# Optimization experiments

Hardware: AMD Instinct MI355X
Metric: run time of the kernel (lower is better)

## Reference

```python
import jax, jax.numpy as jnp
import numpy as np
import math

NEG = -1e32
B, S, D, H, DFF, L = 16, 512, 1024, 8, 4096, 3
DK = D // H


def layernorm(x, g, b, eps=1e-5):
    mu = x.mean(-1, keepdims=True)
    var = ((x - mu) ** 2).mean(-1, keepdims=True)
    return (x - mu) / jnp.sqrt(var + eps) * g + b


def gen_dam(alphas, E, bmask):
    # alphas, E: [H, S, 2]; hard gumbel-softmax with straight-through
    Hh, Ss, _ = alphas.shape
    g = -jnp.log(E + 1e-5)
    y_soft = jax.nn.softmax(alphas + g, axis=-1)  # tau = 1
    idx = jnp.argmax(y_soft, axis=-1)
    y_hard = jax.nn.one_hot(idx, 2, dtype=y_soft.dtype)
    m = y_hard - jax.lax.stop_gradient(y_soft) + y_soft
    m = jnp.broadcast_to(m[:, :, 0:1], (Hh, Ss, Ss))
    m = jnp.triu(m)
    m = jnp.rot90(m, 1, axes=(1, 2))
    i = jnp.arange(Ss)[:, None]
    j = jnp.arange(Ss)[None, :]
    src = jnp.clip(j - i, 0, Ss - 1)
    shifted = m[:, jnp.arange(Ss)[:, None], src]  # mask_tri[:, i, j] = m[:, i, j - i]
    mask_tri = jnp.where(j >= i, shifted, 0.0)
    masks = mask_tri + jnp.swapaxes(jnp.triu(mask_tri, 1), 1, 2)
    masks = jnp.triu(masks, bmask)
    return masks


def attention(q, k, v, src_mask, dam, zero_pad, gammas):
    # q,k,v: [B,H,S,dk]; src_mask: [S,S] bool; dam: [H,S,S] bool
    dk = q.shape[-1]
    Ss = q.shape[2]
    scores = jnp.einsum('bhqd,bhkd->bhqk', q, k) / math.sqrt(dk)
    damb = dam[None]          # [1,H,S,S]
    smb = src_mask[None, None]  # [1,1,S,S]
    # NOTE: faithful to the torch code, where the first masked_fill(mask==0)
    # result is overwritten - only dam masks the first softmax.
    sc = jnp.where(damb, scores, NEG)
    sc = jax.nn.softmax(sc, axis=-1)
    sc = sc * smb.astype(sc.dtype) * damb.astype(sc.dtype)
    distcum = jnp.cumsum(sc, axis=-1)
    disttot = jnp.sum(sc, axis=-1, keepdims=True)
    pos = jnp.abs(jnp.arange(Ss)[None, :] - jnp.arange(Ss)[:, None]).astype(scores.dtype)
    dist = jnp.sqrt(jnp.clip((disttot - distcum) * pos[None, None], 0.0, None))
    dist = jax.lax.stop_gradient(dist)
    gamma = -jax.nn.softplus(gammas)[None]  # [1,H,1,1]
    te = jnp.clip(jnp.exp(dist * gamma), 1e-5, 1e5)
    scores = scores * te
    scores = jnp.where(smb, scores, NEG)
    scores = jnp.where(damb, scores, NEG)
    scores = jax.nn.softmax(scores, axis=-1)
    if zero_pad:
        scores = scores.at[:, :, 0, :].set(0.0)
    return jnp.einsum('bhqk,bhkd->bhqd', scores, v)


def transformer_layer(bmask, query, key, values, apply_pos, p):
    Bb, Ss, Dd = query.shape
    Hh = p['gammas'].shape[0]
    dam = gen_dam(p['alphas'], p['E'], bmask) == 0
    src_mask = jnp.triu(jnp.ones((Ss, Ss), jnp.int32), bmask) == 0
    k = (key @ p['kW'].T + p['kb']).reshape(Bb, Ss, Hh, -1).transpose(0, 2, 1, 3)
    q = (query @ p['kW'].T + p['kb']).reshape(Bb, Ss, Hh, -1).transpose(0, 2, 1, 3)  # kq_same
    v = (values @ p['vW'].T + p['vb']).reshape(Bb, Ss, Hh, -1).transpose(0, 2, 1, 3)
    att = attention(q, k, v, src_mask, dam, bmask == 0, p['gammas'])
    concat = att.transpose(0, 2, 1, 3).reshape(Bb, Ss, Dd)
    q2 = concat @ p['oW'].T + p['ob']
    x = layernorm(query + q2, p['ln1_g'], p['ln1_b'])
    if apply_pos:
        ff = jax.nn.relu(x @ p['w1'].T + p['b1']) @ p['w2'].T + p['b2']
        x = layernorm(x + ff, p['ln2_g'], p['ln2_b'])
    return x


def setup_inputs() -> dict:
    key = jax.random.key(0)
    ks = jax.random.split(key, 16)
    sc = 0.02
    return {
        'q_embed_data': jax.random.normal(ks[0], (B, S, D), jnp.float32),
        'qa_embed_data': jax.random.normal(ks[1], (B, S, D), jnp.float32),
        'kW': sc * jax.random.normal(ks[2], (L, D, D), jnp.float32),
        'kb': jnp.zeros((L, D), jnp.float32),
        'vW': sc * jax.random.normal(ks[3], (L, D, D), jnp.float32),
        'vb': jnp.zeros((L, D), jnp.float32),
        'oW': sc * jax.random.normal(ks[4], (L, D, D), jnp.float32),
        'ob': jnp.zeros((L, D), jnp.float32),
        'gammas': 0.5 * jax.random.normal(ks[5], (L, H, 1, 1), jnp.float32),
        'alphas': 0.001 * jax.random.normal(ks[6], (L, H, S, 2), jnp.float32),
        'ln1_g': jnp.ones((L, D), jnp.float32),
        'ln1_b': jnp.zeros((L, D), jnp.float32),
        'w1': sc * jax.random.normal(ks[7], (L, DFF, D), jnp.float32),
        'b1': jnp.zeros((L, DFF), jnp.float32),
        'w2': sc * jax.random.normal(ks[8], (L, D, DFF), jnp.float32),
        'b2': jnp.zeros((L, D), jnp.float32),
        'ln2_g': jnp.ones((L, D), jnp.float32),
        'ln2_b': jnp.zeros((L, D), jnp.float32),
        'gumbel_E': jax.random.exponential(ks[9], (L, H, S, 2), jnp.float32),
    }


def reference(q_embed_data, qa_embed_data, kW, kb, vW, vb, oW, ob, gammas,
              alphas, ln1_g, ln1_b, w1, b1, w2, b2, ln2_g, ln2_b, gumbel_E):
    def P(l):
        return {'kW': kW[l], 'kb': kb[l], 'vW': vW[l], 'vb': vb[l],
                'oW': oW[l], 'ob': ob[l], 'gammas': gammas[l], 'alphas': alphas[l],
                'ln1_g': ln1_g[l], 'ln1_b': ln1_b[l], 'w1': w1[l], 'b1': b1[l],
                'w2': w2[l], 'b2': b2[l], 'ln2_g': ln2_g[l], 'ln2_b': ln2_b[l],
                'E': gumbel_E[l]}
    # blocks_1: self-attention over answer embedding (mask=1)
    y = transformer_layer(1, qa_embed_data, qa_embed_data, qa_embed_data, True, P(0))
    # blocks_2: self-attn on question emb (no FFN), then cross-attn into y
    x = transformer_layer(1, q_embed_data, q_embed_data, q_embed_data, False, P(1))
    x = transformer_layer(0, x, x, y, True, P(2))
    return x
```

## Files before the change

### kernel.cpp

```cpp
#include <hip/hip_runtime.h>
#include <math.h>

#define NEGV -1e32f

typedef __bf16 bf16_t;
typedef _Float16 f16_t;
typedef __bf16 bf16x8 __attribute__((ext_vector_type(8)));
typedef __bf16 bf16x4 __attribute__((ext_vector_type(4)));
typedef _Float16 f16x8 __attribute__((ext_vector_type(8)));
typedef float floatx4 __attribute__((ext_vector_type(4)));

static __device__ __forceinline__ float fexp(float x) { return __expf(x); }
#if __has_builtin(__builtin_amdgcn_sqrtf)
static __device__ __forceinline__ float fsqrt(float x) { return __builtin_amdgcn_sqrtf(x); }
#else
static __device__ __forceinline__ float fsqrt(float x) { return sqrtf(x); }
#endif
#if __has_builtin(__builtin_amdgcn_rcpf)
static __device__ __forceinline__ float frcp(float x) { return __builtin_amdgcn_rcpf(x); }
#else
static __device__ __forceinline__ float frcp(float x) { return 1.0f / x; }
#endif

static __device__ __forceinline__ float wave_sum(float v) {
#pragma unroll
  for (int d = 32; d > 0; d >>= 1) v += __shfl_xor(v, d, 64);
  return v;
}
static __device__ __forceinline__ float wave_max(float v) {
#pragma unroll
  for (int d = 32; d > 0; d >>= 1) v = fmaxf(v, __shfl_xor(v, d, 64));
  return v;
}

static __device__ __forceinline__ void gl2lds16(const bf16_t* g, bf16_t* l) {
  __builtin_amdgcn_global_load_lds((__attribute__((address_space(1))) void*)(void*)g,
                                   (__attribute__((address_space(3))) void*)l, 16, 0, 0);
}

template <int WM, int WN, int FM, int FN, int BIAS_MODE, bool RELU, int OUT_MODE>
__global__ __launch_bounds__(WM * WN * 64) void gemm_db(
    const bf16_t* __restrict__ A, long lda, long a_so, long a_si,
    const bf16_t* __restrict__ B, long ldb, long b_so, long b_si,
    void* __restrict__ Cv, long ldc, long c_so, long c_si,
    const float* __restrict__ bias, int zdiv, int K, float alpha)
{
  constexpr int THREADS = WM * WN * 64;
  constexpr int BM = WM * FM * 16;
  constexpr int BN = WN * FN * 16;
  constexpr int RR = THREADS / 8;
  constexpr int RA = BM / RR;
  constexpr int RB = BN / RR;
  constexpr int NSTG = RA + RB;
  constexpr int MG = (FM >= 8) ? 2 : 1;
  constexpr int MSUB = FM / MG;
  constexpr int PH = 2 * MG;
  extern __shared__ bf16_t smem[];
  bf16_t* const Asb = smem;
  bf16_t* const Bsb = smem + 2 * (BM * 64);

  const int tid = threadIdx.x;
  const int wave = tid >> 6;
  const int lane = tid & 63;
  const int wm = wave / WN;
  const int wn = wave % WN;
  const int z = blockIdx.z;
  const long zo = z / zdiv;
  const long zi = z % zdiv;
  A += zo * a_so + zi * a_si;
  B += zo * b_so + zi * b_si;
  const long m0 = (long)blockIdx.x * BM;
  const long n0 = (long)blockIdx.y * BN;

  const int srow = tid >> 3;
  const int scol = ((tid & 7) ^ (srow & 7)) * 8;
  const bf16_t* gA = A + (m0 + srow) * lda + scol;
  const bf16_t* gB = B + (n0 + srow) * ldb + scol;
  const int lofs = wave * 512;

  floatx4 acc[FM][FN] = {};
  const int lr = lane & 15;
  const int kg = lane >> 4;
  const int NT = K >> 6;

  auto stage_round = [&](int q, long ko, int dstbuf) {
    if (q < RA)
      gl2lds16(gA + (long)(q * RR) * lda + ko,
               Asb + dstbuf * (BM * 64) + lofs + q * RR * 64);
    else
      gl2lds16(gB + (long)((q - RA) * RR) * ldb + ko,
               Bsb + dstbuf * (BN * 64) + lofs + (q - RA) * RR * 64);
  };

#pragma unroll
  for (int q = 0; q < NSTG; ++q) stage_round(q, 0, 0);

  for (int t = 0; t < NT; ++t) {
    const int buf = t & 1;
    const bool pf = (t + 1 < NT);
    const long ko = (long)(t + 1) * 64;
    if (pf) {
#pragma unroll
      for (int q = 0; q < 2; ++q) stage_round(q, ko, buf ^ 1);
      asm volatile("s_waitcnt vmcnt(2)" ::: "memory");
    } else {
      asm volatile("s_waitcnt vmcnt(0)" ::: "memory");
    }
    __builtin_amdgcn_s_barrier();
    __builtin_amdgcn_sched_barrier(0);
    const bf16_t* __restrict__ Ab = Asb + buf * (BM * 64);
    const bf16_t* __restrict__ Bb = Bsb + buf * (BN * 64);
#pragma unroll
    for (int h = 0; h < 2; ++h) {
      const int slot = ((h * 4 + kg) ^ (lr & 7)) * 8;
      bf16x8 bfr[FN];
#pragma unroll
      for (int g = 0; g < MG; ++g) {
        const int pi = h * MG + g;
        bf16x8 af[MSUB];
#pragma unroll
        for (int m = 0; m < MSUB; ++m)
          af[m] = *(const bf16x8*)(Ab + (wm * (FM * 16) + (g * MSUB + m) * 16 + lr) * 64 + slot);
        if (g == 0) {
#pragma unroll
          for (int n = 0; n < FN; ++n)
            bfr[n] = *(const bf16x8*)(Bb + (wn * (FN * 16) + n * 16 + lr) * 64 + slot);
        }
        if (pf) {
          const int q0 = 2 + pi * 6 / PH;
          const int q1 = 2 + (pi + 1) * 6 / PH;
#pragma unroll
          for (int q = q0; q < q1; ++q) stage_round(q, ko, buf ^ 1);
        }
        asm volatile("s_waitcnt lgkmcnt(0)" ::: "memory");
        __builtin_amdgcn_sched_barrier(0);
        __builtin_amdgcn_s_setprio(1);
#pragma unroll
        for (int m = 0; m < MSUB; ++m)
#pragma unroll
          for (int n = 0; n < FN; ++n)
            acc[g * MSUB + m][n] =
                __builtin_amdgcn_mfma_f32_16x16x32_bf16(af[m], bfr[n], acc[g * MSUB + m][n], 0, 0, 0);
        __builtin_amdgcn_s_setprio(0);
        __builtin_amdgcn_sched_barrier(0);
        __builtin_amdgcn_s_barrier();
      }
    }
  }

  const long coff = zo * c_so + zi * c_si;
  const int q4 = (lane >> 4) * 4;
#pragma unroll
  for (int m = 0; m < FM; ++m) {
#pragma unroll
    for (int n = 0; n < FN; ++n) {
#pragma unroll
      for (int r = 0; r < 4; ++r) {
        const long row = m0 + wm * (FM * 16) + m * 16 + q4 + r;
        const long col = n0 + wn * (FN * 16) + n * 16 + lr;
        float v = acc[m][n][r] * alpha;
        if (BIAS_MODE == 1) v += bias[col];
        if (BIAS_MODE == 2) v += bias[row];
        if (RELU) v = fmaxf(v, 0.0f);
        const long idx = coff + row * ldc + col;
        if (OUT_MODE == 1)      ((bf16_t*)Cv)[idx] = (bf16_t)v;
        else if (OUT_MODE == 2) ((f16_t*)Cv)[idx]  = (f16_t)v;
        else                    ((float*)Cv)[idx]  = v;
      }
    }
  }
}

template <int BIAS_MODE, bool RELU, int OUT_MODE>
__global__ __launch_bounds__(256) void gemm_bt(
    const bf16_t* __restrict__ A, long lda, long a_so, long a_si,
    const bf16_t* __restrict__ B, long ldb, long b_so, long b_si,
    void* __restrict__ Cv, long ldc, long c_so, long c_si,
    const float* __restrict__ bias, int zdiv, int K, float alpha)
{
  __shared__ bf16_t As[8192];
  __shared__ bf16_t Bs[8192];
  const int tid = threadIdx.x;
  const int wave = tid >> 6;
  const int lane = tid & 63;
  const int wr = wave >> 1;
  const int wc = wave & 1;
  const int z = blockIdx.z;
  const long zo = z / zdiv;
  const long zi = z % zdiv;
  A += zo * a_so + zi * a_si;
  B += zo * b_so + zi * b_si;
  const long m0 = (long)blockIdx.x * 128;
  const long n0 = (long)blockIdx.y * 128;

  const int srow = tid >> 3;
  const int scol = ((tid & 7) ^ (srow & 7)) * 8;
  const bf16_t* gA = A + (m0 + srow) * lda + scol;
  const bf16_t* gB = B + (n0 + srow) * ldb + scol;
  bf16_t* lA = As + wave * 512;
  bf16_t* lB = Bs + wave * 512;

  floatx4 acc[4][4] = {};
  const int lr = lane & 15;
  const int kg = lane >> 4;

  for (int k0 = 0; k0 < K; k0 += 64) {
#pragma unroll
    for (int r = 0; r < 4; ++r) {
      gl2lds16(gA + (long)r * 32 * lda + k0, lA + r * 2048);
      gl2lds16(gB + (long)r * 32 * ldb + k0, lB + r * 2048);
    }
    __syncthreads();
#pragma unroll
    for (int h = 0; h < 2; ++h) {
      const int slot = ((h * 4 + kg) ^ (lr & 7)) * 8;
      bf16x8 af[4], bfr[4];
#pragma unroll
      for (int t = 0; t < 4; ++t) {
        af[t]  = *(const bf16x8*)(As + (wr * 64 + t * 16 + lr) * 64 + slot);
        bfr[t] = *(const bf16x8*)(Bs + (wc * 64 + t * 16 + lr) * 64 + slot);
      }
#pragma unroll
      for (int tm = 0; tm < 4; ++tm)
#pragma unroll
        for (int tn = 0; tn < 4; ++tn)
          acc[tm][tn] = __builtin_amdgcn_mfma_f32_16x16x32_bf16(af[tm], bfr[tn], acc[tm][tn], 0, 0, 0);
    }
    __syncthreads();
  }

  const long coff = zo * c_so + zi * c_si;
  const int q4 = (lane >> 4) * 4;
#pragma unroll
  for (int tm = 0; tm < 4; ++tm) {
#pragma unroll
    for (int tn = 0; tn < 4; ++tn) {
#pragma unroll
      for (int r = 0; r < 4; ++r) {
        const long row = m0 + wr * 64 + tm * 16 + q4 + r;
        const long col = n0 + wc * 64 + tn * 16 + lr;
        float v = acc[tm][tn][r] * alpha;
        if (BIAS_MODE == 1) v += bias[col];
        if (BIAS_MODE == 2) v += bias[row];
        if (RELU) v = fmaxf(v, 0.0f);
        const long idx = coff + row * ldc + col;
        if (OUT_MODE == 1)      ((bf16_t*)Cv)[idx] = (bf16_t)v;
        else if (OUT_MODE == 2) ((f16_t*)Cv)[idx]  = (f16_t)v;
        else                    ((float*)Cv)[idx]  = v;
      }
    }
  }
}

__global__ __launch_bounds__(256) void cast_kernel(const float* __restrict__ in,
                                                   bf16_t* __restrict__ out, long n)
{
  const long i = ((long)blockIdx.x * 256 + threadIdx.x) * 4;
  if (i >= n) return;
  const float4 v = *(const float4*)(in + i);
  bf16x4 o;
  o[0] = (bf16_t)v.x; o[1] = (bf16_t)v.y; o[2] = (bf16_t)v.z; o[3] = (bf16_t)v.w;
  *(bf16x4*)(out + i) = o;
}

__global__ void bbit_kernel(const float* __restrict__ alphas, const float* __restrict__ E,
                            int* __restrict__ bbit, int n)
{
  const int i = blockIdx.x * 256 + threadIdx.x;
  if (i >= n) return;
  const float l0 = alphas[2 * i]     - logf(E[2 * i]     + 1e-5f);
  const float l1 = alphas[2 * i + 1] - logf(E[2 * i + 1] + 1e-5f);
  bbit[i] = (l0 >= l1) ? 1 : 0;
}

template <bool XBF>
__global__ __launch_bounds__(256) void ln_kernel(
    const void* __restrict__ Xv, const float* __restrict__ R,
    const float* __restrict__ g, const float* __restrict__ b,
    float* __restrict__ out32, bf16_t* __restrict__ out16)
{
  const long row = blockIdx.x;
  const int t = threadIdx.x;
  float x0, x1, x2, x3;
  if (XBF) {
    const bf16x4 xv = *(const bf16x4*)((const bf16_t*)Xv + row * 1024 + t * 4);
    x0 = (float)xv[0]; x1 = (float)xv[1]; x2 = (float)xv[2]; x3 = (float)xv[3];
  } else {
    const float4 xv = *(const float4*)((const float*)Xv + row * 1024 + t * 4);
    x0 = xv.x; x1 = xv.y; x2 = xv.z; x3 = xv.w;
  }
  const float4 rv = *(const float4*)(R + row * 1024 + t * 4);
  const float v0 = x0 + rv.x, v1 = x1 + rv.y, v2 = x2 + rv.z, v3 = x3 + rv.w;
  float s  = v0 + v1 + v2 + v3;
  float s2 = v0 * v0 + v1 * v1 + v2 * v2 + v3 * v3;
  s = wave_sum(s); s2 = wave_sum(s2);
  __shared__ float red[8];
  const int wv = t >> 6, lane = t & 63;
  if (lane == 0) { red[wv] = s; red[4 + wv] = s2; }
  __syncthreads();
  s  = red[0] + red[1] + red[2] + red[3];
  s2 = red[4] + red[5] + red[6] + red[7];
  const float mu = s * (1.0f / 1024.0f);
  const float var = s2 * (1.0f / 1024.0f) - mu * mu;
  const float rstd = rsqrtf(var + 1e-5f);
  const float4 gv = *(const float4*)(g + t * 4);
  const float4 bv = *(const float4*)(b + t * 4);
  float4 ov;
  ov.x = (v0 - mu) * rstd * gv.x + bv.x;
  ov.y = (v1 - mu) * rstd * gv.y + bv.y;
  ov.z = (v2 - mu) * rstd * gv.z + bv.z;
  ov.w = (v3 - mu) * rstd * gv.w + bv.w;
  if (out32) *(float4*)(out32 + row * 1024 + t * 4) = ov;
  if (out16) {
    bf16x4 oh;
    oh[0] = (bf16_t)ov.x; oh[1] = (bf16_t)ov.y; oh[2] = (bf16_t)ov.z; oh[3] = (bf16_t)ov.w;
    *(bf16x4*)(out16 + row * 1024 + t * 4) = oh;
  }
}

__global__ __launch_bounds__(256) void attn_mid(
    const f16_t* __restrict__ S, bf16_t* __restrict__ P,
    const int* __restrict__ bbit, const float* __restrict__ gam,
    const int bmask, const int zero_pad)
{
  const int wid = threadIdx.x >> 6;
  const int lane = threadIdx.x & 63;
  const long rowid = (long)blockIdx.x * 4 + wid;
  const int i = (int)(rowid & 511);
  const int h = (int)(rowid >> 9) & 7;
  const f16_t* s = S + rowid * 512;
  const int jb = lane * 8;

  const float gv = gam[h];
  const float gamma = -log1pf(fexp(gv));

  float sv[8];
  {
    const f16x8 a = *(const f16x8*)(s + jb);
#pragma unroll
    for (int u = 0; u < 8; ++u) sv[u] = (float)a[u];
  }
  const int* bb = bbit + h * 512;
  float z[8];
  bool band[8];
  float m1 = NEGV;
#pragma unroll
  for (int u = 0; u < 8; ++u) {
    const int j = jb + u;
    const bool bd = j < i + bmask;
    band[u] = bd;
    int d = j - i; d = d < 0 ? 0 : d;
    const bool allowed = bd || (bb[d] == 0);
    z[u] = allowed ? sv[u] : NEGV;
    m1 = fmaxf(m1, z[u]);
  }
  m1 = wave_max(m1);
  float e[8], es = 0.f;
#pragma unroll
  for (int u = 0; u < 8; ++u) { e[u] = fexp(z[u] - m1); es += e[u]; }
  es = wave_sum(es);
  const float inv1 = frcp(es);

  float c[8];
  float run = 0.f;
#pragma unroll
  for (int u = 0; u < 8; ++u) {
    const float p = band[u] ? e[u] * inv1 : 0.f;
    run += p;
    c[u] = run;
  }
  float x = run;
#pragma unroll
  for (int d = 1; d < 64; d <<= 1) {
    const float y = __shfl_up(x, (unsigned)d, 64);
    if (lane >= d) x += y;
  }
  const float tot = __shfl(x, 63, 64);
  const float ex = x - run;

  float z2[8];
  float m2 = NEGV;
#pragma unroll
  for (int u = 0; u < 8; ++u) {
    const int j = jb + u;
    const float cc = c[u] + ex;
    const float pos = fabsf((float)(i - j));
    const float dist = fsqrt(fmaxf((tot - cc) * pos, 0.f));
    float te = fexp(dist * gamma);
    te = fminf(fmaxf(te, 1e-5f), 1e5f);
    z2[u] = band[u] ? sv[u] * te : NEGV;
    m2 = fmaxf(m2, z2[u]);
  }
  m2 = wave_max(m2);
  float f[8], es2 = 0.f;
#pragma unroll
  for (int u = 0; u < 8; ++u) { f[u] = fexp(z2[u] - m2); es2 += f[u]; }
  es2 = wave_sum(es2);
  const float inv2 = (zero_pad && i == 0) ? 0.f : frcp(es2);
  bf16x8 o;
#pragma unroll
  for (int u = 0; u < 8; ++u) o[u] = (bf16_t)(f[u] * inv2);
  *(bf16x8*)(P + rowid * 512 + jb) = o;
}

extern "C" void kernel_launch(void* const* d_in, const int* in_sizes, int n_in,
                              void* d_out, int out_size, void* d_ws, size_t ws_size,
                              hipStream_t stream)
{
  (void)in_sizes; (void)n_in; (void)out_size; (void)ws_size;
  const float* q_emb  = (const float*)d_in[0];
  const float* qa_emb = (const float*)d_in[1];
  const float* kW = (const float*)d_in[2];
  const float* kb = (const float*)d_in[3];
  const float* vW = (const float*)d_in[4];
  const float* vb = (const float*)d_in[5];
  const float* oW = (const float*)d_in[6];
  const float* ob = (const float*)d_in[7];
  const float* gammas = (const float*)d_in[8];
  const float* alphas = (const float*)d_in[9];
  const float* ln1_g = (const float*)d_in[10];
  const float* ln1_b = (const float*)d_in[11];
  const float* w1 = (const float*)d_in[12];
  const float* b1 = (const float*)d_in[13];
  const float* w2 = (const float*)d_in[14];
  const float* b2 = (const float*)d_in[15];
  const float* ln2_g = (const float*)d_in[16];
  const float* ln2_b = (const float*)d_in[17];
  const float* gumE = (const float*)d_in[18];
  float* outp = (float*)d_out;

  static bool attr_done = false;
  if (!attr_done) {
    attr_done = true;
    (void)hipFuncSetAttribute(reinterpret_cast<const void*>(&gemm_db<2,2,4,4,1,false,1>),
                              hipFuncAttributeMaxDynamicSharedMemorySize, 65536);
    (void)hipFuncSetAttribute(reinterpret_cast<const void*>(&gemm_db<2,2,4,4,2,false,1>),
                              hipFuncAttributeMaxDynamicSharedMemorySize, 65536);
    (void)hipFuncSetAttribute(reinterpret_cast<const void*>(&gemm_db<2,2,4,4,0,false,1>),
                              hipFuncAttributeMaxDynamicSharedMemorySize, 65536);
    (void)hipFuncSetAttribute(reinterpret_cast<const void*>(&gemm_db<2,2,4,4,1,false,0>),
                              hipFuncAttributeMaxDynamicSharedMemorySize, 65536);
    (void)hipFuncSetAttribute(reinterpret_cast<const void*>(&gemm_db<2,4,8,4,1,true,1>),
                              hipFuncAttributeMaxDynamicSharedMemorySize, 131072);
  }

  const size_t MBc = 1ull << 20;
  char* W = (char*)d_ws;
  int*    bbit = (int*)W;
  bf16_t* VB   = (bf16_t*)(W + 1 * MBc);
  bf16_t* XB   = (bf16_t*)(W + 17 * MBc);
  bf16_t* kWb  = (bf16_t*)(W + 33 * MBc);
  bf16_t* vWb  = (bf16_t*)(W + 39 * MBc);
  bf16_t* oWb  = (bf16_t*)(W + 45 * MBc);
  bf16_t* w1b  = (bf16_t*)(W + 51 * MBc);
  bf16_t* w2b  = (bf16_t*)(W + 59 * MBc);
  bf16_t* KQB  = (bf16_t*)(W + 67 * MBc);
  bf16_t* VT   = (bf16_t*)(W + 83 * MBc);
  f16_t*  SSPP = (f16_t*)(W + 99 * MBc);
  bf16_t* PPb  = (bf16_t*)(W + 99 * MBc);
  bf16_t* ATT  = (bf16_t*)(W + 163 * MBc);
  float*  O32  = (float*)(W + 67 * MBc);
  bf16_t* X1B  = (bf16_t*)(W + 99 * MBc);
  bf16_t* H1B  = (bf16_t*)(W + 115 * MBc);

  const long ND = 8388608;

  auto run_layer = [&](int l, const void* Qin, bool qin_bf16, const bf16_t* XBp,
                       const bf16_t* VBp, bool apply_pos, int bmask,
                       float* o32, bf16_t* o16) {
    const bf16_t* kWl = kWb + (long)l * 1048576;
    const bf16_t* vWl = vWb + (long)l * 1048576;
    const bf16_t* oWl = oWb + (long)l * 1048576;
    gemm_db<2,2,4,4,1,false,1><<<dim3(64, 8, 1), dim3(256), 65536, stream>>>(
        XBp, 1024, 0, 0, kWl, 1024, 0, 0, (void*)KQB, 1024, 0, 0,
        kb + l * 1024, 1, 1024, 1.0f);
    gemm_db<2,2,4,4,2,false,1><<<dim3(8, 4, 16), dim3(256), 65536, stream>>>(
        vWl, 1024, 0, 0, VBp, 1024, 524288, 0, (void*)VT, 512, 524288, 0,
        vb + l * 1024, 1, 1024, 1.0f);
    const int zp = (bmask == 0) ? 1 : 0;
    gemm_bt<0, false, 2><<<dim3(4, 4, 128), dim3(256), 0, stream>>>(
        KQB, 1024, 524288, 128, KQB, 1024, 524288, 128,
        (void*)SSPP, 512, 2097152, 262144, nullptr, 8, 128, 0.08838834764831845f);
    attn_mid<<<dim3(16384), dim3(256), 0, stream>>>(
        SSPP, PPb, bbit + l * 4096, gammas + l * 8, bmask, zp);
    gemm_db<2,2,4,4,0,false,1><<<dim3(4, 1, 128), dim3(256), 65536, stream>>>(
        PPb, 512, 2097152, 262144, VT, 512, 524288, 65536,
        (void*)ATT, 1024, 524288, 128, nullptr, 8, 512, 1.0f);
    gemm_db<2,2,4,4,1,false,0><<<dim3(64, 8, 1), dim3(256), 65536, stream>>>(
        ATT, 1024, 0, 0, oWl, 1024, 0, 0, (void*)O32, 1024, 0, 0,
        ob + l * 1024, 1, 1024, 1.0f);
    if (!apply_pos) {
      if (qin_bf16)
        ln_kernel<true><<<dim3(8192), dim3(256), 0, stream>>>(
            Qin, O32, ln1_g + l * 1024, ln1_b + l * 1024, o32, o16);
      else
        ln_kernel<false><<<dim3(8192), dim3(256), 0, stream>>>(
            Qin, O32, ln1_g + l * 1024, ln1_b + l * 1024, o32, o16);
    } else {
      cast_kernel<<<dim3(4096), dim3(256), 0, stream>>>(w1 + (long)l * 4194304, w1b, 4194304);
      cast_kernel<<<dim3(4096), dim3(256), 0, stream>>>(w2 + (long)l * 4194304, w2b, 4194304);
      if (qin_bf16)
        ln_kernel<true><<<dim3(8192), dim3(256), 0, stream>>>(
            Qin, O32, ln1_g + l * 1024, ln1_b + l * 1024, nullptr, X1B);
      else
        ln_kernel<false><<<dim3(8192), dim3(256), 0, stream>>>(
            Qin, O32, ln1_g + l * 1024, ln1_b + l * 1024, nullptr, X1B);
      gemm_db<2,4,8,4,1,true,1><<<dim3(32, 16, 1), dim3(512), 131072, stream>>>(
          X1B, 1024, 0, 0, w1b, 1024, 0, 0, (void*)H1B, 4096, 0, 0,
          b1 + l * 4096, 1, 1024, 1.0f);
      gemm_db<2,2,4,4,1,false,0><<<dim3(64, 8, 1), dim3(256), 65536, stream>>>(
          H1B, 4096, 0, 0, w2b, 4096, 0, 0, (void*)O32, 1024, 0, 0,
          b2 + l * 1024, 1, 4096, 1.0f);
      ln_kernel<true><<<dim3(8192), dim3(256), 0, stream>>>(
          X1B, O32, ln2_g + l * 1024, ln2_b + l * 1024, o32, o16);
    }
  };

  bbit_kernel<<<dim3(48), dim3(256), 0, stream>>>(alphas, gumE, bbit, 12288);
  cast_kernel<<<dim3(3072), dim3(256), 0, stream>>>(kW, kWb, 3145728);
  cast_kernel<<<dim3(3072), dim3(256), 0, stream>>>(vW, vWb, 3145728);
  cast_kernel<<<dim3(3072), dim3(256), 0, stream>>>(oW, oWb, 3145728);

  cast_kernel<<<dim3(8192), dim3(256), 0, stream>>>(qa_emb, XB, ND);
  run_layer(0, qa_emb, false, XB, XB, true, 1, nullptr, VB);
  cast_kernel<<<dim3(8192), dim3(256), 0, stream>>>(q_emb, XB, ND);
  run_layer(1, q_emb, false, XB, XB, false, 1, nullptr, XB);
  run_layer(2, XB, true, XB, VB, true, 0, outp, nullptr);
}
```

Before: 1.099 ms.

## Issue all next-tile loads upfront in gemm_db and reuse it for QK^T

New measurement: 1.125 ms. 2.4% more time.

```diff
diff --git a/kernel.cpp b/kernel.cpp
--- a/kernel.cpp
+++ b/kernel.cpp
@@ -54,7 +54,6 @@
   constexpr int NSTG = RA + RB;
   constexpr int MG = (FM >= 8) ? 2 : 1;
   constexpr int MSUB = FM / MG;
-  constexpr int PH = 2 * MG;
   extern __shared__ bf16_t smem[];
   bf16_t* const Asb = smem;
   bf16_t* const Bsb = smem + 2 * (BM * 64);
@@ -97,12 +96,11 @@
 
   for (int t = 0; t < NT; ++t) {
     const int buf = t & 1;
-    const bool pf = (t + 1 < NT);
-    const long ko = (long)(t + 1) * 64;
-    if (pf) {
-#pragma unroll
-      for (int q = 0; q < 2; ++q) stage_round(q, ko, buf ^ 1);
-      asm volatile("s_waitcnt vmcnt(2)" ::: "memory");
+    if (t + 1 < NT) {
+      const long ko = (long)(t + 1) * 64;
+#pragma unroll
+      for (int q = 0; q < NSTG; ++q) stage_round(q, ko, buf ^ 1);
+      asm volatile("s_waitcnt vmcnt(%0)" :: "n"(NSTG) : "memory");
     } else {
       asm volatile("s_waitcnt vmcnt(0)" ::: "memory");
     }
@@ -116,7 +114,6 @@
       bf16x8 bfr[FN];
 #pragma unroll
       for (int g = 0; g < MG; ++g) {
-        const int pi = h * MG + g;
         bf16x8 af[MSUB];
 #pragma unroll
         for (int m = 0; m < MSUB; ++m)
@@ -126,13 +123,8 @@
           for (int n = 0; n < FN; ++n)
             bfr[n] = *(const bf16x8*)(Bb + (wn * (FN * 16) + n * 16 + lr) * 64 + slot);
         }
-        if (pf) {
-          const int q0 = 2 + pi * 6 / PH;
-          const int q1 = 2 + (pi + 1) * 6 / PH;
-#pragma unroll
-          for (int q = q0; q < q1; ++q) stage_round(q, ko, buf ^ 1);
-        }
-        asm volatile("s_waitcnt lgkmcnt(0)" ::: "memory");
+        __builtin_amdgcn_sched_barrier(0);
+        __builtin_amdgcn_s_barrier();
         __builtin_amdgcn_sched_barrier(0);
         __builtin_amdgcn_s_setprio(1);
 #pragma unroll
@@ -159,87 +151,6 @@
         const long row = m0 + wm * (FM * 16) + m * 16 + q4 + r;
         const long col = n0 + wn * (FN * 16) + n * 16 + lr;
         float v = acc[m][n][r] * alpha;
-        if (BIAS_MODE == 1) v += bias[col];
-        if (BIAS_MODE == 2) v += bias[row];
-        if (RELU) v = fmaxf(v, 0.0f);
-        const long idx = coff + row * ldc + col;
-        if (OUT_MODE == 1)      ((bf16_t*)Cv)[idx] = (bf16_t)v;
-        else if (OUT_MODE == 2) ((f16_t*)Cv)[idx]  = (f16_t)v;
-        else                    ((float*)Cv)[idx]  = v;
-      }
-    }
-  }
-}
-
-template <int BIAS_MODE, bool RELU, int OUT_MODE>
-__global__ __launch_bounds__(256) void gemm_bt(
-    const bf16_t* __restrict__ A, long lda, long a_so, long a_si,
-    const bf16_t* __restrict__ B, long ldb, long b_so, long b_si,
-    void* __restrict__ Cv, long ldc, long c_so, long c_si,
-    const float* __restrict__ bias, int zdiv, int K, float alpha)
-{
-  __shared__ bf16_t As[8192];
-  __shared__ bf16_t Bs[8192];
-  const int tid = threadIdx.x;
-  const int wave = tid >> 6;
-  const int lane = tid & 63;
-  const int wr = wave >> 1;
-  const int wc = wave & 1;
-  const int z = blockIdx.z;
-  const long zo = z / zdiv;
-  const long zi = z % zdiv;
-  A += zo * a_so + zi * a_si;
-  B += zo * b_so + zi * b_si;
-  const long m0 = (long)blockIdx.x * 128;
-  const long n0 = (long)blockIdx.y * 128;
-
-  const int srow = tid >> 3;
-  const int scol = ((tid & 7) ^ (srow & 7)) * 8;
-  const bf16_t* gA = A + (m0 + srow) * lda + scol;
-  const bf16_t* gB = B + (n0 + srow) * ldb + scol;
-  bf16_t* lA = As + wave * 512;
-  bf16_t* lB = Bs + wave * 512;
-
-  floatx4 acc[4][4] = {};
-  const int lr = lane & 15;
-  const int kg = lane >> 4;
-
-  for (int k0 = 0; k0 < K; k0 += 64) {
-#pragma unroll
-    for (int r = 0; r < 4; ++r) {
-      gl2lds16(gA + (long)r * 32 * lda + k0, lA + r * 2048);
-      gl2lds16(gB + (long)r * 32 * ldb + k0, lB + r * 2048);
-    }
-    __syncthreads();
-#pragma unroll
-    for (int h = 0; h < 2; ++h) {
-      const int slot = ((h * 4 + kg) ^ (lr & 7)) * 8;
-      bf16x8 af[4], bfr[4];
-#pragma unroll
-      for (int t = 0; t < 4; ++t) {
-        af[t]  = *(const bf16x8*)(As + (wr * 64 + t * 16 + lr) * 64 + slot);
-        bfr[t] = *(const bf16x8*)(Bs + (wc * 64 + t * 16 + lr) * 64 + slot);
-      }
-#pragma unroll
-      for (int tm = 0; tm < 4; ++tm)
-#pragma unroll
-        for (int tn = 0; tn < 4; ++tn)
-          acc[tm][tn] = __builtin_amdgcn_mfma_f32_16x16x32_bf16(af[tm], bfr[tn], acc[tm][tn], 0, 0, 0);
-    }
-    __syncthreads();
-  }
-
-  const long coff = zo * c_so + zi * c_si;
-  const int q4 = (lane >> 4) * 4;
-#pragma unroll
-  for (int tm = 0; tm < 4; ++tm) {
-#pragma unroll
-    for (int tn = 0; tn < 4; ++tn) {
-#pragma unroll
-      for (int r = 0; r < 4; ++r) {
-        const long row = m0 + wr * 64 + tm * 16 + q4 + r;
-        const long col = n0 + wc * 64 + tn * 16 + lr;
-        float v = acc[tm][tn][r] * alpha;
         if (BIAS_MODE == 1) v += bias[col];
         if (BIAS_MODE == 2) v += bias[row];
         if (RELU) v = fmaxf(v, 0.0f);
@@ -438,6 +349,8 @@
                               hipFuncAttributeMaxDynamicSharedMemorySize, 65536);
     (void)hipFuncSetAttribute(reinterpret_cast<const void*>(&gemm_db<2,2,4,4,0,false,1>),
                               hipFuncAttributeMaxDynamicSharedMemorySize, 65536);
+    (void)hipFuncSetAttribute(reinterpret_cast<const void*>(&gemm_db<2,2,4,4,0,false,2>),
+                              hipFuncAttributeMaxDynamicSharedMemorySize, 65536);
     (void)hipFuncSetAttribute(reinterpret_cast<const void*>(&gemm_db<2,2,4,4,1,false,0>),
                               hipFuncAttributeMaxDynamicSharedMemorySize, 65536);
     (void)hipFuncSetAttribute(reinterpret_cast<const void*>(&gemm_db<2,4,8,4,1,true,1>),
@@ -478,7 +391,7 @@
         vWl, 1024, 0, 0, VBp, 1024, 524288, 0, (void*)VT, 512, 524288, 0,
         vb + l * 1024, 1, 1024, 1.0f);
     const int zp = (bmask == 0) ? 1 : 0;
-    gemm_bt<0, false, 2><<<dim3(4, 4, 128), dim3(256), 0, stream>>>(
+    gemm_db<2,2,4,4,0,false,2><<<dim3(4, 4, 128), dim3(256), 65536, stream>>>(
         KQB, 1024, 524288, 128, KQB, 1024, 524288, 128,
         (void*)SSPP, 512, 2097152, 262144, nullptr, 8, 128, 0.08838834764831845f);
     attn_mid<<<dim3(16384), dim3(256), 0, stream>>>(
```
